# Kernel tuning notes

Hardware: AMD Instinct MI355X
Metric: run time of the kernel (lower is better)

Reference implementation:

```python
import jax, jax.numpy as jnp
import numpy as np

B, NV, NDIRS, NRINGS, NCH, NF = 2, 15000, 16, 3, 32, 64


def setup_inputs() -> dict:
    key = jax.random.key(0)
    k1, k2, k3, k4 = jax.random.split(key, 4)
    y = jax.random.normal(k1, (B, NV, NDIRS, NCH), dtype=jnp.float32)
    ft_v = jax.random.randint(k2, (NV, NRINGS, NDIRS), 0, NV, dtype=jnp.int32)
    ft_d = jax.random.randint(k3, (NV, NRINGS, NDIRS), 0, NDIRS, dtype=jnp.int32)
    kernel = jax.random.normal(k4, (NRINGS, NDIRS, NCH, NF), dtype=jnp.float32) * 0.05
    bias = jnp.zeros((NF,), dtype=jnp.float32)
    return {"y": y, "ft_v": ft_v, "ft_d": ft_d, "kernel": kernel, "bias": bias}


def reference(y, ft_v, ft_d, kernel, bias):
    # y: [b, nv, ndirs, nch]; ft_v/ft_d: [nv, nrings, ndirs]; kernel: [nrings, ndirs, nch, nf]
    b, nv, ndirs, nch = y.shape
    f = jnp.transpose(y, (1, 2, 3, 0))  # [nv, ndirs, nch, b]
    dirs = jnp.arange(ndirs)

    def per_dir(l):
        # cyclic forward shift of the direction axis, composed with the
        # frame-transporter gather: z[v,r,d,c,b] = f[ft_v[v,r,d], (ft_d[v,r,d]+l)%n, c, b]
        d_idx = (ft_d + l) % ndirs                # [nv, nrings, ndirs]
        z = f[ft_v, d_idx]                        # [nv, nrings, ndirs, nch, b]
        # kernel shifted in reverse: k_l[:, d] = kernel[:, (d-l)%n]
        k_l = kernel[:, (dirs - l) % ndirs]       # [nrings, ndirs, nch, nf]
        return jnp.einsum('vrdcb,rdcf->vbf', z, k_l)  # [nv, b, nf]

    out = jax.lax.map(per_dir, dirs)              # [ndirs, nv, b, nf] (sequential, like tf.while_loop)
    out = jnp.transpose(out, (2, 1, 0, 3))        # [b, nv, ndirs, nf]
    out = out + bias
    return jax.nn.relu(out)
```

## Files before the change

### kernel.cpp

```cpp
#include <hip/hip_runtime.h>

#define NV 15000
#define ND 16
#define NR 3
#define NC 32
#define NFDIM 64
#define BB 2

typedef short bf16x8 __attribute__((ext_vector_type(8)));
typedef float f32x4 __attribute__((ext_vector_type(4)));
typedef unsigned short u16x8 __attribute__((ext_vector_type(8)));

#define KB_OFF     30720000u
#define WS_NEEDED  30916608u

__device__ __forceinline__ unsigned short f2bf(float x) {
  union { float f; unsigned int u; } cv; cv.f = x;
  unsigned int u = cv.u;
  u += 0x7FFF + ((u >> 16) & 1);
  return (unsigned short)(u >> 16);
}

__global__ void prep_y(const float* __restrict__ y, u16x8* __restrict__ yt) {
  int tid = blockIdx.x * 256 + threadIdx.x;
  if (tid >= (NV * ND * BB * NC) / 8) return;
  int o   = tid * 8;
  int v   = o >> 10;
  int rem = o & 1023;
  int d   = rem >> 6;
  int b   = (rem >> 5) & 1;
  int c0  = rem & 31;
  const f32x4* src = (const f32x4*)(y + (((b * NV + v) * ND + d) * NC + c0));
  f32x4 lo = src[0], hi = src[1];
  u16x8 r;
#pragma unroll
  for (int i = 0; i < 4; i++) { r[i] = f2bf(lo[i]); r[4 + i] = f2bf(hi[i]); }
  yt[tid] = r;
}

__global__ void prep_kb(const float* __restrict__ kern, unsigned short* __restrict__ kb) {
  int t = blockIdx.x * 256 + threadIdx.x;
  if (t >= 48 * 4 * 64) return;
  int lane  = t & 63;
  int ft    = (t >> 6) & 3;
  int chunk = t >> 8;
  int q = lane >> 4;
  int f = (lane & 15) * 4 + ft;
  unsigned short* dst = kb + t * 8;
#pragma unroll
  for (int j = 0; j < 8; j++) {
    int k = q * 8 + j;
    dst[j] = f2bf(kern[(chunk * NC + k) * NFDIM + f]);
  }
}

__global__ __launch_bounds__(256, 3) void sync_conv_main(
    const unsigned short* __restrict__ yt, const unsigned short* __restrict__ kb,
    const int* __restrict__ ftv, const int* __restrict__ ftd,
    const float* __restrict__ bias, float* __restrict__ out) {
  __shared__ int pidx_lds[16][49];

  int tid  = threadIdx.x;
  int lane = tid & 63;
  int mg   = blockIdx.x >> 2;
  int lg   = blockIdx.x & 3;
  int l    = lg * 4 + (tid >> 6);
  int vbase = mg * 16;

  for (int t = tid; t < 16 * 48; t += 256) {
    int i = t / 48, j = t - i * 48;
    int v = vbase + i; v = v < NV ? v : NV - 1;
    pidx_lds[i][j] = ftv[v * 48 + j] * 16 + (ftd[v * 48 + j] & 15);
  }
  __syncthreads();

  int q    = lane >> 4;
  int n    = lane & 15;
  int b    = n & 1;
  int voff = n >> 1;
  int lane_elem = b * 32 + q * 8;
  const unsigned short* kb_lane = kb + lane * 8;

  f32x4 acc[2][4];
#pragma unroll
  for (int i = 0; i < 2; i++)
#pragma unroll
    for (int j = 0; j < 4; j++) acc[i][j] = (f32x4){0.f, 0.f, 0.f, 0.f};

  bf16x8 bufA[2][2][2];
  bf16x8 bufB[2][2][4];

  auto load_batch = [&](int bidx, int par) {
    int k0 = bidx * 2;
#pragma unroll
    for (int ds = 0; ds < 2; ds++) {
      int k = k0 + ds;
      int r = k >> 4;
      int dp = ((k & 15) - l) & 15;
      const unsigned short* kbp = kb_lane + (r * 16 + dp) * 2048;
#pragma unroll
      for (int ft = 0; ft < 4; ft++)
        bufB[par][ds][ft] = *reinterpret_cast<const bf16x8*>(kbp + ft * 512);
#pragma unroll
      for (int mt = 0; mt < 2; mt++) {
        int p  = pidx_lds[mt * 8 + voff][k];
        int dd = ((p & 15) + l) & 15;
        int off = (p >> 4) * 1024 + (dd << 6) + lane_elem;
        bufA[par][mt][ds] = *reinterpret_cast<const bf16x8*>(yt + off);
      }
    }
  };
  auto compute_batch = [&](int par) {
#pragma unroll
    for (int ds = 0; ds < 2; ds++)
#pragma unroll
      for (int mt = 0; mt < 2; mt++)
#pragma unroll
        for (int ft = 0; ft < 4; ft++)
          acc[mt][ft] = __builtin_amdgcn_mfma_f32_16x16x32_bf16(
              bufA[par][mt][ds], bufB[par][ds][ft], acc[mt][ft], 0, 0, 0);
  };

  load_batch(0, 0);
  for (int i = 0; i < 12; i++) {
    load_batch(2 * i + 1, 1);
    compute_batch(0);
    if (i < 11) load_batch(2 * i + 2, 0);
    compute_batch(1);
  }

  f32x4 bv = *reinterpret_cast<const f32x4*>(bias + 4 * n);

#pragma unroll
  for (int mt = 0; mt < 2; mt++) {
#pragma unroll
    for (int reg = 0; reg < 4; reg++) {
      int m  = q * 4 + reg;
      int v  = vbase + mt * 8 + (m >> 1);
      int bb = m & 1;
      if (v < NV) {
        f32x4 x;
#pragma unroll
        for (int ft = 0; ft < 4; ft++) {
          float t = acc[mt][ft][reg] + bv[ft];
          x[ft] = t > 0.f ? t : 0.f;
        }
        float* dst = out + (((bb * NV + v) * ND + l) * NFDIM) + 4 * n;
        __builtin_nontemporal_store(x, (f32x4*)dst);
      }
    }
  }
}

__global__ void fallback_kernel(const float* __restrict__ y, const int* __restrict__ ftv,
                                const int* __restrict__ ftd, const float* __restrict__ kern,
                                const float* __restrict__ bias, float* __restrict__ out) {
  int idx = blockIdx.x;
  int l = idx & 15;
  int v = (idx >> 4) % NV;
  int b = idx / (NV * ND);
  int f = threadIdx.x;
  float acc = 0.f;
  for (int r = 0; r < NR; r++)
    for (int d = 0; d < ND; d++) {
      int ii = (v * NR + r) * ND + d;
      int vv = ftv[ii];
      int dd = (ftd[ii] + l) & 15;
      int dp = (d - l) & 15;
      const float* yp = y + ((b * NV + vv) * ND + dd) * NC;
      const float* kp = kern + ((r * 16 + dp) * NC) * NFDIM + f;
#pragma unroll 8
      for (int c = 0; c < NC; c++) acc += yp[c] * kp[c * NFDIM];
    }
  float x = acc + bias[f];
  out[idx * NFDIM + f] = x > 0.f ? x : 0.f;
}

extern "C" void kernel_launch(void* const* d_in, const int* in_sizes, int n_in,
                              void* d_out, int out_size, void* d_ws, size_t ws_size,
                              hipStream_t stream) {
  const float* y    = (const float*)d_in[0];
  const int*   ftv  = (const int*)d_in[1];
  const int*   ftd  = (const int*)d_in[2];
  const float* kern = (const float*)d_in[3];
  const float* bias = (const float*)d_in[4];
  float* out = (float*)d_out;

  if (ws_size >= (size_t)WS_NEEDED) {
    char* ws = (char*)d_ws;
    unsigned short* yt = (unsigned short*)ws;
    unsigned short* kb = (unsigned short*)(ws + KB_OFF);

    prep_y<<<(NV * ND * BB * NC / 8 + 255) / 256, 256, 0, stream>>>(y, (u16x8*)yt);
    prep_kb<<<(48 * 4 * 64 + 255) / 256, 256, 0, stream>>>(kern, kb);
    sync_conv_main<<<3752, 256, 0, stream>>>(yt, kb, ftv, ftd, bias, out);
  } else {
    fallback_kernel<<<BB * NV * ND, NFDIM, 0, stream>>>(y, ftv, ftd, kern, bias, out);
  }
}
```

Measured before the change: 376.1 us.

## Double vertices per block to reuse kernel fragments across four M-tiles

```diff
diff --git a/kernel.cpp b/kernel.cpp
--- a/kernel.cpp
+++ b/kernel.cpp
@@ -58,16 +58,16 @@
     const unsigned short* __restrict__ yt, const unsigned short* __restrict__ kb,
     const int* __restrict__ ftv, const int* __restrict__ ftd,
     const float* __restrict__ bias, float* __restrict__ out) {
-  __shared__ int pidx_lds[16][49];
+  __shared__ int pidx_lds[32][49];
 
   int tid  = threadIdx.x;
   int lane = tid & 63;
   int mg   = blockIdx.x >> 2;
   int lg   = blockIdx.x & 3;
   int l    = lg * 4 + (tid >> 6);
-  int vbase = mg * 16;
+  int vbase = mg * 32;
 
-  for (int t = tid; t < 16 * 48; t += 256) {
+  for (int t = tid; t < 32 * 48; t += 256) {
     int i = t / 48, j = t - i * 48;
     int v = vbase + i; v = v < NV ? v : NV - 1;
     pidx_lds[i][j] = ftv[v * 48 + j] * 16 + (ftd[v * 48 + j] & 15);
@@ -81,58 +81,51 @@
   int lane_elem = b * 32 + q * 8;
   const unsigned short* kb_lane = kb + lane * 8;
 
-  f32x4 acc[2][4];
+  f32x4 acc[4][4];
 #pragma unroll
-  for (int i = 0; i < 2; i++)
+  for (int i = 0; i < 4; i++)
 #pragma unroll
     for (int j = 0; j < 4; j++) acc[i][j] = (f32x4){0.f, 0.f, 0.f, 0.f};
 
-  bf16x8 bufA[2][2][2];
-  bf16x8 bufB[2][2][4];
+  bf16x8 bufA[2][4];
+  bf16x8 bufB[2][4];
 
-  auto load_batch = [&](int bidx, int par) {
-    int k0 = bidx * 2;
+  auto load_step = [&](int k, int par) {
+    int r  = k >> 4;
+    int dp = ((k & 15) - l) & 15;
+    const unsigned short* kbp = kb_lane + (r * 16 + dp) * 2048;
 #pragma unroll
-    for (int ds = 0; ds < 2; ds++) {
-      int k = k0 + ds;
-      int r = k >> 4;
-      int dp = ((k & 15) - l) & 15;
-      const unsigned short* kbp = kb_lane + (r * 16 + dp) * 2048;
+    for (int ft = 0; ft < 4; ft++)
+      bufB[par][ft] = *reinterpret_cast<const bf16x8*>(kbp + ft * 512);
+#pragma unroll
+    for (int mt = 0; mt < 4; mt++) {
+      int p  = pidx_lds[mt * 8 + voff][k];
+      int dd = ((p & 15) + l) & 15;
+      int off = (p >> 4) * 1024 + (dd << 6) + lane_elem;
+      bufA[par][mt] = *reinterpret_cast<const bf16x8*>(yt + off);
+    }
+  };
+  auto compute_step = [&](int par) {
+#pragma unroll
+    for (int mt = 0; mt < 4; mt++)
 #pragma unroll
       for (int ft = 0; ft < 4; ft++)
-        bufB[par][ds][ft] = *reinterpret_cast<const bf16x8*>(kbp + ft * 512);
-#pragma unroll
-      for (int mt = 0; mt < 2; mt++) {
-        int p  = pidx_lds[mt * 8 + voff][k];
-        int dd = ((p & 15) + l) & 15;
-        int off = (p >> 4) * 1024 + (dd << 6) + lane_elem;
-        bufA[par][mt][ds] = *reinterpret_cast<const bf16x8*>(yt + off);
-      }
-    }
-  };
-  auto compute_batch = [&](int par) {
-#pragma unroll
-    for (int ds = 0; ds < 2; ds++)
-#pragma unroll
-      for (int mt = 0; mt < 2; mt++)
-#pragma unroll
-        for (int ft = 0; ft < 4; ft++)
-          acc[mt][ft] = __builtin_amdgcn_mfma_f32_16x16x32_bf16(
-              bufA[par][mt][ds], bufB[par][ds][ft], acc[mt][ft], 0, 0, 0);
+        acc[mt][ft] = __builtin_amdgcn_mfma_f32_16x16x32_bf16(
+            bufA[par][mt], bufB[par][ft], acc[mt][ft], 0, 0, 0);
   };
 
-  load_batch(0, 0);
-  for (int i = 0; i < 12; i++) {
-    load_batch(2 * i + 1, 1);
-    compute_batch(0);
-    if (i < 11) load_batch(2 * i + 2, 0);
-    compute_batch(1);
+  load_step(0, 0);
+#pragma unroll 2
+  for (int k = 0; k < 47; k++) {
+    load_step(k + 1, (k + 1) & 1);
+    compute_step(k & 1);
   }
+  compute_step(47 & 1);
 
   f32x4 bv = *reinterpret_cast<const f32x4*>(bias + 4 * n);
 
 #pragma unroll
-  for (int mt = 0; mt < 2; mt++) {
+  for (int mt = 0; mt < 4; mt++) {
 #pragma unroll
     for (int reg = 0; reg < 4; reg++) {
       int m  = q * 4 + reg;
@@ -193,7 +186,7 @@
 
     prep_y<<<(NV * ND * BB * NC / 8 + 255) / 256, 256, 0, stream>>>(y, (u16x8*)yt);
     prep_kb<<<(48 * 4 * 64 + 255) / 256, 256, 0, stream>>>(kern, kb);
-    sync_conv_main<<<3752, 256, 0, stream>>>(yt, kb, ftv, ftd, bias, out);
+    sync_conv_main<<<1876, 256, 0, stream>>>(yt, kb, ftv, ftd, bias, out);
   } else {
     fallback_kernel<<<BB * NV * ND, NFDIM, 0, stream>>>(y, ftv, ftd, kern, bias, out);
   }
```

Result: slower. 386.0 us (+2.6%).
